# Kernel tuning notes

Measured on AMD Instinct MI355X. Metric: run time of the kernel, lower is better.

The kernel has to match this reference:

```python
import jax, jax.numpy as jnp
import numpy as np

N, E, G = 50000, 800000, 64
IN, H, ED, OUT = 32, 96, 16, 128
EPS_GEN = 1e-7   # GENConv message eps
EPS_BN = 1e-5    # BatchNorm1d eps


def _bn(x, g, b):
    # training-mode BatchNorm1d: batch stats, biased variance
    mu = jnp.mean(x, axis=0)
    var = jnp.var(x, axis=0)
    return (x - mu) * jax.lax.rsqrt(var + EPS_BN) * g + b


def _genconv(x_src, x_dst, src, dst, ea, mw1, mg, mb, mw2):
    # message: relu(x_j + e_ij) + eps            [E, H]
    msg = jax.nn.relu(x_src[src] + ea) + EPS_GEN
    n = x_dst.shape[0]
    # softmax aggregation over incoming edges per dst node (t=1.0)
    m = jax.ops.segment_max(msg, dst, num_segments=n)
    ex = jnp.exp(msg - m[dst])
    s = jax.ops.segment_sum(ex, dst, num_segments=n)
    agg = jax.ops.segment_sum(msg * (ex / s[dst]), dst, num_segments=n)
    h = agg + x_dst
    # GENConv internal MLP: Lin(H,2H,no bias) -> BN -> ReLU -> Lin(2H,H,no bias)
    h = jax.nn.relu(_bn(h @ mw1, mg, mb))
    return h @ mw2


def _forward(x, edge_attr, w_src1, w_dst1, w_edge1,
             mlp1_w1, mlp1_g, mlp1_b, mlp1_w2, bn1_g, bn1_b,
             w_edge2, mlp2_w1, mlp2_g, mlp2_b, mlp2_w2, bn2_g, bn2_b,
             w_edge3, mlp3_w1, mlp3_g, mlp3_b, mlp3_w2, bn3_g, bn3_b,
             lin_w, lin_b, edge_index, batch):
    src, dst = edge_index[0], edge_index[1]
    h = _genconv(x @ w_src1, x @ w_dst1, src, dst, edge_attr @ w_edge1,
                 mlp1_w1, mlp1_g, mlp1_b, mlp1_w2)
    h = jax.nn.relu(_bn(h, bn1_g, bn1_b))
    h = _genconv(h, h, src, dst, edge_attr @ w_edge2,
                 mlp2_w1, mlp2_g, mlp2_b, mlp2_w2)
    h = jax.nn.relu(_bn(h, bn2_g, bn2_b))
    h = _genconv(h, h, src, dst, edge_attr @ w_edge3,
                 mlp3_w1, mlp3_g, mlp3_b, mlp3_w2)
    h = jax.nn.relu(_bn(h, bn3_g, bn3_b))
    # global mean pool over graphs (dropout is identity in eval)
    cnt = jax.ops.segment_sum(jnp.ones((h.shape[0],), h.dtype), batch, num_segments=G)
    pooled = jax.ops.segment_sum(h, batch, num_segments=G) / jnp.maximum(cnt, 1.0)[:, None]
    return pooled @ lin_w + lin_b


def setup_inputs() -> dict:
    key = jax.random.key(0)
    ks = jax.random.split(key, 20)
    rn = lambda i, shp, s=0.05: jax.random.normal(ks[i], shp, jnp.float32) * s
    return {
        'x': rn(0, (N, IN), 1.0),
        'edge_attr': rn(1, (E, ED), 1.0),
        'edge_index': jax.random.randint(ks[2], (2, E), 0, N, jnp.int32),
        'batch': jnp.sort(jax.random.randint(ks[3], (N,), 0, G, jnp.int32)),
        'w_src1': rn(4, (IN, H)), 'w_dst1': rn(5, (IN, H)), 'w_edge1': rn(6, (ED, H)),
        'mlp1_w1': rn(7, (H, 2 * H)), 'mlp1_g': jnp.ones(2 * H), 'mlp1_b': jnp.zeros(2 * H),
        'mlp1_w2': rn(8, (2 * H, H)), 'bn1_g': jnp.ones(H), 'bn1_b': jnp.zeros(H),
        'w_edge2': rn(9, (ED, H)),
        'mlp2_w1': rn(10, (H, 2 * H)), 'mlp2_g': jnp.ones(2 * H), 'mlp2_b': jnp.zeros(2 * H),
        'mlp2_w2': rn(11, (2 * H, H)), 'bn2_g': jnp.ones(H), 'bn2_b': jnp.zeros(H),
        'w_edge3': rn(12, (ED, H)),
        'mlp3_w1': rn(13, (H, 2 * H)), 'mlp3_g': jnp.ones(2 * H), 'mlp3_b': jnp.zeros(2 * H),
        'mlp3_w2': rn(14, (2 * H, H)), 'bn3_g': jnp.ones(H), 'bn3_b': jnp.zeros(H),
        'lin_w': rn(15, (H, OUT)), 'lin_b': jnp.zeros(OUT),
    }


def reference(x, edge_attr, edge_index, batch, w_src1, w_dst1, w_edge1,
              mlp1_w1, mlp1_g, mlp1_b, mlp1_w2, bn1_g, bn1_b,
              w_edge2, mlp2_w1, mlp2_g, mlp2_b, mlp2_w2, bn2_g, bn2_b,
              w_edge3, mlp3_w1, mlp3_g, mlp3_b, mlp3_w2, bn3_g, bn3_b,
              lin_w, lin_b):
    return _forward(x, edge_attr, w_src1, w_dst1, w_edge1,
                    mlp1_w1, mlp1_g, mlp1_b, mlp1_w2, bn1_g, bn1_b,
                    w_edge2, mlp2_w1, mlp2_g, mlp2_b, mlp2_w2, bn2_g, bn2_b,
                    w_edge3, mlp3_w1, mlp3_g, mlp3_b, mlp3_w2, bn3_g, bn3_b,
                    lin_w, lin_b, edge_index, batch)
```

## Files before the change

### kernel.cpp

```cpp
#include <hip/hip_runtime.h>
#include <math.h>

#define NN 50000
#define EE 800000
#define GG 64
#define HH 96
#define H2 192
#define INF 32
#define EDF 16
#define OUTF 128
#define EPS_GEN 1e-7f
#define EPS_BN 1e-5f
#define NPB 100
#define NB_SCAN 49
#define NBH (256 * NB_SCAN)
#define BSCAN_PT 13
#define LOG2E 1.44269504088896f
#define SHIFT2 28.85390081777927f

typedef _Float16 f16;
typedef _Float16 f16x2 __attribute__((ext_vector_type(2)));
typedef _Float16 f16x8 __attribute__((ext_vector_type(8)));
typedef float f32x4 __attribute__((ext_vector_type(4)));

static inline size_t align256(size_t x) { return (x + 255) & ~(size_t)255; }

__device__ __forceinline__ float fdot2(f16x2 a, f16x2 b, float c) {
#if __has_builtin(__builtin_amdgcn_fdot2)
    return __builtin_amdgcn_fdot2(a, b, c, false);
#else
    return fmaf((float)a.x, (float)b.x, fmaf((float)a.y, (float)b.y, c));
#endif
}

__device__ __forceinline__ float exp2fast(float x) {
#if __has_builtin(__builtin_amdgcn_exp2f)
    return __builtin_amdgcn_exp2f(x);
#else
    return exp2f(x);
#endif
}

union W8 { float4 f[2]; f16x2 h[8]; };
union EAu { float4 f; f16x2 h[4]; };
union XUu { float2 f; f16x2 h[2]; };

__device__ __forceinline__ void agg_step(const EAu& e0, const EAu& e1, const XUu& xu,
                                         const W8* w, float* num, float* den) {
    float xv[4] = {(float)xu.h[0].x, (float)xu.h[0].y, (float)xu.h[1].x, (float)xu.h[1].y};
    #pragma unroll
    for (int cc = 0; cc < 4; ++cc) {
        float acc = 0.f;
        #pragma unroll
        for (int k = 0; k < 4; ++k) acc = fdot2(e0.h[k], w[cc].h[k], acc);
        #pragma unroll
        for (int k = 0; k < 4; ++k) acc = fdot2(e1.h[k], w[cc].h[4 + k], acc);
        float msg = fmaxf(xv[cc] + acc, 0.f) + EPS_GEN;
        float p = exp2fast(fmaf(msg, LOG2E, -SHIFT2));
        den[cc] += p;
        num[cc] = fmaf(msg, p, num[cc]);
    }
}


__global__ __launch_bounds__(256) void hist_kernel(const int* __restrict__ dst,
                                                   int* __restrict__ deg) {
    int e = blockIdx.x * 256 + threadIdx.x;
    if (e >= EE) return;
    atomicAdd(&deg[dst[e]], 1);
}

__global__ __launch_bounds__(1024) void scan1_kernel(const int* __restrict__ deg,
                                                     int* __restrict__ offs,
                                                     int* __restrict__ bsum,
                                                     int* __restrict__ bhist) {
    __shared__ int ws[16];
    __shared__ int lh[256];
    int tid = threadIdx.x, lane = tid & 63, w = tid >> 6;
    if (tid < 256) lh[tid] = 0;
    int i = blockIdx.x * 1024 + tid;
    int v = (i < NN) ? deg[i] : 0;
    __syncthreads();
    if (i < NN) {
        int b = 255 - (v > 255 ? 255 : v);
        atomicAdd(&lh[b], 1);
    }
    int x = v;
    #pragma unroll
    for (int off = 1; off < 64; off <<= 1) {
        int y = __shfl_up(x, off, 64);
        if (lane >= off) x += y;
    }
    if (lane == 63) ws[w] = x;
    __syncthreads();
    int wpre = 0;
    for (int j = 0; j < w; ++j) wpre += ws[j];
    if (i < NN) offs[i] = wpre + x - v;
    if (tid == 1023) bsum[blockIdx.x] = wpre + x;
    if (tid < 256) bhist[tid * NB_SCAN + blockIdx.x] = lh[tid];
}

__global__ __launch_bounds__(1024) void bscan_kernel(int* __restrict__ bhist,
// ... 30 lines not shown
    }
    if (lane == 63) ws[w] = x;
    __syncthreads();
    int wpre = 0;
    for (int j = 0; j < w; ++j) wpre += ws[j];
    int pre = wpre + x - s;
    #pragma unroll
    for (int i = 0; i < BSCAN_PT; ++i) {
        int idx = base + i;
        if (idx < NBH) bhist[idx] = pre + loc[i];
    }
}

__global__ __launch_bounds__(1024) void finsort_kernel(int* __restrict__ offs,
                                                       const int* __restrict__ bsum,
                                                       const int* __restrict__ deg,
                                                       const int* __restrict__ bhist,
                                                       int* __restrict__ perm) {
    __shared__ int cnt[256];
    int tid = threadIdx.x;
    if (tid < 256) cnt[tid] = 0;
    __syncthreads();
    int n = blockIdx.x * 1024 + tid;
    if (n < NN) {
        offs[n] += bsum[blockIdx.x];
        int d = deg[n];
        int b = 255 - (d > 255 ? 255 : d);
        int rank = atomicAdd(&cnt[b], 1);
        perm[bhist[b * NB_SCAN + blockIdx.x] + rank] = n;
    }
    if (n == NN) offs[NN] = EE;
}

__global__ __launch_bounds__(256) void scatter_kernel(const int* __restrict__ src,
                                                      const int* __restrict__ dst,
                                                      const int* __restrict__ offs,
                                                      int* __restrict__ cnt2,
                                                      const float* __restrict__ eattr,
                                                      int* __restrict__ csr_src,
                                                      float4* __restrict__ csrea) {
    int e = blockIdx.x * 256 + threadIdx.x;
    if (e >= EE) return;
    int d = dst[e];
    int slot = offs[d] + atomicAdd(&cnt2[d], 1);
    csr_src[slot] = src[e];
    const float4* ep = (const float4*)(eattr + (size_t)e * EDF);
    float4 v0 = ep[0], v1 = ep[1], v2 = ep[2], v3 = ep[3];
    union { f16x2 h[4]; float4 f; } a, b;
    a.h[0] = f16x2{(f16)v0.x, (f16)v0.y};
    a.h[1] = f16x2{(f16)v0.z, (f16)v0.w};
    a.h[2] = f16x2{(f16)v1.x, (f16)v1.y};
    a.h[3] = f16x2{(f16)v1.z, (f16)v1.w};
    b.h[0] = f16x2{(f16)v2.x, (f16)v2.y};
    b.h[1] = f16x2{(f16)v2.z, (f16)v2.w};
    b.h[2] = f16x2{(f16)v3.x, (f16)v3.y};
    b.h[3] = f16x2{(f16)v3.z, (f16)v3.w};
    csrea[(size_t)slot * 2] = a.f;
    csrea[(size_t)slot * 2 + 1] = b.f;
}

__global__ __launch_bounds__(256) void wprep_kernel(
    const float* __restrict__ we0, const float* __restrict__ we1, const float* __restrict__ we2,
    const float* __restrict__ m10, const float* __restrict__ m11, const float* __restrict__ m12,
    const float* __restrict__ m20, const float* __restrict__ m21, const float* __restrict__ m22,
    f16* __restrict__ wte, f16* __restrict__ wt1, f16* __restrict__ wt2,
    int* __restrict__ csr_src) {
    int idx = blockIdx.x * 256 + threadIdx.x;
    if (idx < 8) csr_src[EE + idx] = 0;
    if (idx < 4608) {
        const float* w = (idx < 1536) ? we0 : ((idx < 3072) ? we1 : we2);
        int r = idx % 1536, c = r / EDF, k = r % EDF;
        wte[idx] = (f16)w[k * HH + c];
    } else if (idx < 4608 + 3 * 18432) {
        int m = idx - 4608;
        const float* w = (m < 18432) ? m10 : ((m < 36864) ? m11 : m12);
        int r = m % 18432, j = r / HH, k = r % HH;
        wt1[m] = (f16)w[k * H2 + j];
    } else if (idx < 4608 + 6 * 18432) {
        int m = idx - 4608 - 3 * 18432;
        const float* w = (m < 18432) ? m20 : ((m < 36864) ? m21 : m22);
        int r = m % 18432, j = r / H2, k = r % H2;
        wt2[m] = (f16)w[k * HH + j];
    }
}


__global__ __launch_bounds__(256) void proj_kernel(const float* __restrict__ x,
                                                   const float* __restrict__ ws,
                                                   const float* __restrict__ wd,
                                                   f16* __restrict__ xs,
                                                   f16* __restrict__ xd) {
    __shared__ float Ws[INF * HH], Wd[INF * HH];
    int tid = threadIdx.x;
    for (int i = tid; i < INF * HH; i += 256) { Ws[i] = ws[i]; Wd[i] = wd[i]; }
    __syncthreads();
    int gid = blockIdx.x * 256 + tid;
    if (gid >= NN * HH) return;
    int n = gid / HH, c = gid % HH;
    const float* xr = x + (size_t)n * INF;
    float as = 0.f, ad = 0.f;
    #pragma unroll
    for (int k = 0; k < INF; ++k) {
        float xv = xr[k];
        as = fmaf(xv, Ws[k * HH + c], as);
        ad = fmaf(xv, Wd[k * HH + c], ad);
    }
    xs[gid] = (f16)as;
    xd[gid] = (f16)ad;
}


#define AGG_LOAD(E0, E1, XU, JJ, SR)                                    \
    E0.f = csrea[(size_t)(JJ) * 2];                                     \
    E1.f = csrea[(size_t)(JJ) * 2 + 1];                                 \
    XU.f = *(const float2*)(xsrc + (size_t)(SR) * HH + c0);

__global__ __launch_bounds__(192) void agg_kernel(const f16* __restrict__ xsrc,
                                                  const f16* __restrict__ xdst,
                                                  const float4* __restrict__ csrea,
                                                  const f16* __restrict__ wt,
                                                  const int* __restrict__ offs,
                                                  const int* __restrict__ csr_src,
                                                  const int* __restrict__ perm,
                                                  float* __restrict__ stats,
                                                  f16* __restrict__ hpre) {
    int tid = threadIdx.x;
    if (blockIdx.x == 0) {
        for (int t = tid; t < 576; t += 192) stats[t] = 0.f;
    }
    int idx = blockIdx.x * 8 + tid / 24;
    if (idx >= NN) return;
    int node = perm[idx];
    int cg = tid % 24, c0 = cg * 4;
    W8 w[4];
    #pragma unroll
    for (int cc = 0; cc < 4; ++cc) {
        const float4* wp = (const float4*)(wt + (c0 + cc) * EDF);
        w[cc].f[0] = wp[0];
        w[cc].f[1] = wp[1];
    }
    XUu xd;
    xd.f = *(const float2*)(xdst + (size_t)node * HH + c0);
    int s0 = offs[node], s1 = offs[node + 1];
    float num[4] = {0.f, 0.f, 0.f, 0.f}, den[4] = {0.f, 0.f, 0.f, 0.f};
    if (s0 < s1) {
        int last = s1 - 1;
        EAu eA0, eA1, eB0, eB1, eC0, eC1;
        XUu xA, xB, xC;
        int sA = csr_src[s0], sB = csr_src[s0 + 1], sC = csr_src[s0 + 2];
        AGG_LOAD(eA0, eA1, xA, s0, sA)
        AGG_LOAD(eB0, eB1, xB, s0 + 1, sB)
        AGG_LOAD(eC0, eC1, xC, s0 + 2, sC)
        int sD = csr_src[s0 + 3], sE = csr_src[s0 + 4], sF = csr_src[s0 + 5];
        for (int j = s0; j < s1; j += 3) {
            agg_step(eA0, eA1, xA, w, num, den);
            AGG_LOAD(eA0, eA1, xA, j + 3, sD)
            sD = csr_src[j + 6];
            if (j + 1 <= last) agg_step(eB0, eB1, xB, w, num, den);
            AGG_LOAD(eB0, eB1, xB, j + 4, sE)
            sE = csr_src[j + 7];
            if (j + 2 <= last) agg_step(eC0, eC1, xC, w, num, den);
            AGG_LOAD(eC0, eC1, xC, j + 5, sF)
            sF = csr_src[j + 8];
        }
    }
    float xdv[4] = {(float)xd.h[0].x, (float)xd.h[0].y, (float)xd.h[1].x, (float)xd.h[1].y};
    float r0 = (den[0] > 0.f) ? num[0] / den[0] : 0.f;
    float r1 = (den[1] > 0.f) ? num[1] / den[1] : 0.f;
    float r2 = (den[2] > 0.f) ? num[2] / den[2] : 0.f;
    float r3 = (den[3] > 0.f) ? num[3] / den[3] : 0.f;
    union { float2 f; f16x2 h[2]; } o;
    o.h[0] = f16x2{(f16)(r0 + xdv[0]), (f16)(r1 + xdv[1])};
    o.h[1] = f16x2{(f16)(r2 + xdv[2]), (f16)(r3 + xdv[3])};
    *(float2*)(hpre + (size_t)node * HH + c0) = o.f;
}

#define LDA1 104

__global__ __launch_bounds__(256) void gemm1_kernel(const f16* __restrict__ A,
                                                    const f16* __restrict__ Wt,
                                                    f16* __restrict__ T,
                                                    float* __restrict__ colsum,
                                                    float* __restrict__ colsumsq) {
    __shared__ f16 Al[64 * LDA1];
    __shared__ f16 Wl[192 * LDA1];
    __shared__ float red[H2 * 2];
    int tid = threadIdx.x, n0 = blockIdx.x * 64;
    for (int v = tid; v < 64 * 12; v += 256) {
        int r = v / 12, c8 = (v % 12) * 8;
        float4 d = {0.f, 0.f, 0.f, 0.f};
        if (n0 + r < NN) d = *(const float4*)(A + (size_t)(n0 + r) * HH + c8);
        *(float4*)(Al + r * LDA1 + c8) = d;
    }
    for (int v = tid; v < 192 * 12; v += 256) {
        int r = v / 12, c8 = (v % 12) * 8;
        *(float4*)(Wl + r * LDA1 + c8) = *(const float4*)(Wt + r * HH + c8);
    }
    if (tid < H2) { red[tid] = 0.f; red[H2 + tid] = 0.f; }
    __syncthreads();
    int wv = tid >> 6, l = tid & 63, lr = l & 15, lg = l >> 4;
    int i0 = wv * 16;
    f32x4 acc[12];
    #pragma unroll
    for (int t = 0; t < 12; ++t) acc[t] = (f32x4){0.f, 0.f, 0.f, 0.f};
    #pragma unroll
    for (int ks = 0; ks < 3; ++ks) {
        int k0 = ks * 32 + lg * 8;
        f16x8 af = *(const f16x8*)(Al + (i0 + lr) * LDA1 + k0);
        #pragma unroll
        for (int t = 0; t < 12; ++t) {
            f16x8 bf = *(const f16x8*)(Wl + (t * 16 + lr) * LDA1 + k0);
            acc[t] = __builtin_amdgcn_mfma_f32_16x16x32_f16(af, bf, acc[t], 0, 0, 0);
        }
    }
    #pragma unroll
    for (int t = 0; t < 12; ++t) {
        int col = t * 16 + lr;
        float s = 0.f, q = 0.f;
        #pragma unroll
        for (int rr = 0; rr < 4; ++rr) {
            int row = n0 + i0 + lg * 4 + rr;
            float v = acc[t][rr];
            if (row < NN) {
                T[(size_t)row * H2 + col] = (f16)v;
                s += v;
                q = fmaf(v, v, q);
            }
        }
        s += __shfl_xor(s, 16); s += __shfl_xor(s, 32);
        q += __shfl_xor(q, 16); q += __shfl_xor(q, 32);
        if (lg == 0) { atomicAdd(&red[col], s); atomicAdd(&red[H2 + col], q); }
    }
    __syncthreads();
    if (tid < H2) {
        atomicAdd(&colsum[tid], red[tid]);
        atomicAdd(&colsumsq[tid], red[H2 + tid]);
    }
}

#define LDA2 200

__global__ __launch_bounds__(256) void gemm2_kernel(const f16* __restrict__ T,
                                                    const f16* __restrict__ Wt,
                                                    const float* __restrict__ cs1,
                                                    const float* __restrict__ cq1,
                                                    const float* __restrict__ g1,
                                                    const float* __restrict__ b1,
                                                    f16* __restrict__ U,
                                                    float* __restrict__ colsum,
                                                    float* __restrict__ colsumsq) {
    __shared__ f16 Al[64 * LDA2];
    __shared__ f16 Wl[96 * LDA2];
    __shared__ float ab[H2 * 2];
    __shared__ float red[HH * 2];
    int tid = threadIdx.x, n0 = blockIdx.x * 64;
    if (tid < H2) {
        const float invN = 1.f / (float)NN;
        float mu = cs1[tid] * invN;
        float var = fmaxf(cq1[tid] * invN - mu * mu, 0.f);
        float a = g1[tid] * rsqrtf(var + EPS_BN);
        ab[tid] = a;
        ab[H2 + tid] = b1[tid] - mu * a;
    }
    if (tid < HH) { red[tid] = 0.f; red[HH + tid] = 0.f; }
    __syncthreads();
    for (int v = tid; v < 64 * 24; v += 256) {
        int r = v / 24, c8 = (v % 24) * 8;
        float4 dd = {0.f, 0.f, 0.f, 0.f};
        if (n0 + r < NN) {
            union { float4 f; f16x2 h[4]; } u, o;
            u.f = *(const float4*)(T + (size_t)(n0 + r) * H2 + c8);
            #pragma unroll
            for (int p = 0; p < 4; ++p) {
                float x0 = fmaxf(fmaf((float)u.h[p].x, ab[c8 + 2 * p], ab[H2 + c8 + 2 * p]), 0.f);
                float x1 = fmaxf(fmaf((float)u.h[p].y, ab[c8 + 2 * p + 1], ab[H2 + c8 + 2 * p + 1]), 0.f);
                o.h[p] = f16x2{(f16)x0, (f16)x1};
            }
            dd = o.f;
        }
        *(float4*)(Al + r * LDA2 + c8) = dd;
    }
    for (int v = tid; v < 96 * 24; v += 256) {
        int r = v / 24, c8 = (v % 24) * 8;
        *(float4*)(Wl + r * LDA2 + c8) = *(const float4*)(Wt + r * H2 + c8);
    }
    __syncthreads();
    int wv = tid >> 6, l = tid & 63, lr = l & 15, lg = l >> 4;
    int i0 = wv * 16;
    f32x4 acc[6];
    #pragma unroll
    for (int t = 0; t < 6; ++t) acc[t] = (f32x4){0.f, 0.f, 0.f, 0.f};
    #pragma unroll
    for (int ks = 0; ks < 6; ++ks) {
        int k0 = ks * 32 + lg * 8;
        f16x8 af = *(const f16x8*)(Al + (i0 + lr) * LDA2 + k0);
        #pragma unroll
        for (int t = 0; t < 6; ++t) {
            f16x8 bf = *(const f16x8*)(Wl + (t * 16 + lr) * LDA2 + k0);
            acc[t] = __builtin_amdgcn_mfma_f32_16x16x32_f16(af, bf, acc[t], 0, 0, 0);
        }
    }
    #pragma unroll
    for (int t = 0; t < 6; ++t) {
        int col = t * 16 + lr;
        float s = 0.f, q = 0.f;
        #pragma unroll
        for (int rr = 0; rr < 4; ++rr) {
            int row = n0 + i0 + lg * 4 + rr;
            float v = acc[t][rr];
            if (row < NN) {
                U[(size_t)row * HH + col] = (f16)v;
                s += v;
                q = fmaf(v, v, q);
            }
        }
        s += __shfl_xor(s, 16); s += __shfl_xor(s, 32);
        q += __shfl_xor(q, 16); q += __shfl_xor(q, 32);
        if (lg == 0) { atomicAdd(&red[col], s); atomicAdd(&red[HH + col], q); }
    }
    __syncthreads();
    if (tid < HH) {
        atomicAdd(&colsum[tid], red[tid]);
        atomicAdd(&colsumsq[tid], red[HH + tid]);
    }
}


__global__ __launch_bounds__(256) void elem_kernel(const f16* __restrict__ U,
                                                   const float* __restrict__ cs2,
                                                   const float* __restrict__ cq2,
                                                   const float* __restrict__ g2,
                                                   const float* __restrict__ b2,
                                                   f16* __restrict__ Hout) {
    __shared__ float ab[HH * 2];
    int tid = threadIdx.x;
    if (tid < HH) {
        const float invN = 1.f / (float)NN;
        float mu = cs2[tid] * invN;
        float var = fmaxf(cq2[tid] * invN - mu * mu, 0.f);
        float a = g2[tid] * rsqrtf(var + EPS_BN);
        ab[tid] = a;
        ab[HH + tid] = b2[tid] - mu * a;
    }
    __syncthreads();
    int i = blockIdx.x * 256 + tid;
    if (i >= NN * HH / 8) return;
    union { float4 f; f16x2 h[4]; } u, o;
    u.f = ((const float4*)U)[i];
    int k = (i % 12) * 8;
    #pragma unroll
    for (int p = 0; p < 4; ++p) {
        float x0 = fmaxf(fmaf((float)u.h[p].x, ab[k + 2 * p], ab[HH + k + 2 * p]), 0.f);
        float x1 = fmaxf(fmaf((float)u.h[p].y, ab[k + 2 * p + 1], ab[HH + k + 2 * p + 1]), 0.f);
// ... 54 lines not shown
    float inv = 1.f / fmaxf((float)(lo - s), 1.f);
    float acc = lb[o];
    for (int c = 0; c < HH; ++c) acc = fmaf(pool[g * HH + c] * inv, lw[c * OUTF + o], acc);
    out[(size_t)g * OUTF + o] = acc;
}


extern "C" void kernel_launch(void* const* d_in, const int* in_sizes, int n_in,
                              void* d_out, int out_size, void* d_ws, size_t ws_size,
                              hipStream_t stream) {
    const float* x = (const float*)d_in[0];
    const float* eattr = (const float*)d_in[1];
    const int* eidx = (const int*)d_in[2];
    const int* batch = (const int*)d_in[3];
    const float* w_src1 = (const float*)d_in[4];
    const float* w_dst1 = (const float*)d_in[5];
    const float* w_e[3] = {(const float*)d_in[6], (const float*)d_in[13], (const float*)d_in[20]};
    const float* mw1[3] = {(const float*)d_in[7], (const float*)d_in[14], (const float*)d_in[21]};
    const float* mg[3] = {(const float*)d_in[8], (const float*)d_in[15], (const float*)d_in[22]};
    const float* mb[3] = {(const float*)d_in[9], (const float*)d_in[16], (const float*)d_in[23]};
    const float* mw2[3] = {(const float*)d_in[10], (const float*)d_in[17], (const float*)d_in[24]};
    const float* bng[3] = {(const float*)d_in[11], (const float*)d_in[18], (const float*)d_in[25]};
    const float* bnb[3] = {(const float*)d_in[12], (const float*)d_in[19], (const float*)d_in[26]};
    const float* lin_w = (const float*)d_in[27];
    const float* lin_b = (const float*)d_in[28];
    float* out = (float*)d_out;

    const int* src = eidx;
    const int* dst = eidx + EE;

    char* base = (char*)d_ws;
    size_t off = 0;
    int* deg = (int*)(base + off); off = align256(off + (size_t)NN * 4);
    int* cnt2 = (int*)(base + off); off = align256(off + (size_t)NN * 4);
    size_t degcnt_span = off;
    int* offs = (int*)(base + off); off = align256(off + (size_t)(NN + 1) * 4);
    int* bsum = (int*)(base + off); off = align256(off + (size_t)NB_SCAN * 4);
    int* bhist = (int*)(base + off); off = align256(off + (size_t)NBH * 4);
    int* perm = (int*)(base + off); off = align256(off + (size_t)NN * 4);
    int* csr_src = (int*)(base + off); off = align256(off + (size_t)(EE + 8) * 4);
    float* stats = (float*)(base + off); off = align256(off + 576 * 4);
    float* colsum1 = stats;
    float* colsumsq1 = stats + 192;
    float* colsum2 = stats + 384;
    float* colsumsq2 = stats + 480;
    float* pool = (float*)(base + off); off = align256(off + (size_t)GG * HH * 4);
    f16* wte = (f16*)(base + off); off = align256(off + (size_t)3 * 1536 * 2);
    f16* wt1 = (f16*)(base + off); off = align256(off + (size_t)3 * 18432 * 2);
    f16* wt2 = (f16*)(base + off); off = align256(off + (size_t)3 * 18432 * 2);
    f16* XS = (f16*)(base + off); off = align256(off + (size_t)NN * HH * 2);
    f16* XD = (f16*)(base + off); off = align256(off + (size_t)NN * HH * 2);
    f16* HP = (f16*)(base + off); off = align256(off + (size_t)NN * HH * 2);
    f16* T = (f16*)(base + off); off = align256(off + (size_t)NN * H2 * 2);
    float4* csrea = (float4*)(base + off); off = align256(off + (size_t)(EE + 8) * 32);
    (void)in_sizes; (void)n_in; (void)out_size; (void)ws_size;

    hipMemsetAsync(deg, 0, degcnt_span, stream);
    hist_kernel<<<(EE + 255) / 256, 256, 0, stream>>>(dst, deg);
    scan1_kernel<<<NB_SCAN, 1024, 0, stream>>>(deg, offs, bsum, bhist);
    bscan_kernel<<<1, 1024, 0, stream>>>(bhist, bsum, pool);
    finsort_kernel<<<NB_SCAN, 1024, 0, stream>>>(offs, bsum, deg, bhist, perm);
    scatter_kernel<<<(EE + 255) / 256, 256, 0, stream>>>(src, dst, offs, cnt2, eattr,
                                                         csr_src, csrea);
    wprep_kernel<<<(4608 + 6 * 18432 + 255) / 256, 256, 0, stream>>>(
        w_e[0], w_e[1], w_e[2], mw1[0], mw1[1], mw1[2], mw2[0], mw2[1], mw2[2],
        wte, wt1, wt2, csr_src);

    proj_kernel<<<(NN * HH + 255) / 256, 256, 0, stream>>>(x, w_src1, w_dst1, XS, XD);

    for (int l = 0; l < 3; ++l) {
        const f16* xdst = (l == 0) ? XD : XS;
        agg_kernel<<<(NN + 7) / 8, 192, 0, stream>>>(XS, xdst, csrea, wte + l * 1536, offs,
                                                     csr_src, perm, stats, HP);
        gemm1_kernel<<<(NN + 63) / 64, 256, 0, stream>>>(HP, wt1 + l * 18432, T,
                                                         colsum1, colsumsq1);
        gemm2_kernel<<<(NN + 63) / 64, 256, 0, stream>>>(T, wt2 + l * 18432, colsum1,
                                                         colsumsq1, mg[l], mb[l], HP,
                                                         colsum2, colsumsq2);
        if (l < 2)
            elem_kernel<<<(NN * HH / 8 + 255) / 256, 256, 0, stream>>>(HP, colsum2, colsumsq2,
                                                                       bng[l], bnb[l], XS);
    }

    pool_bn_kernel<<<(NN + NPB - 1) / NPB, 192, 0, stream>>>(HP, colsum2, colsumsq2,
                                                             bng[2], bnb[2], batch, pool);
    out_kernel<<<GG, 128, 0, stream>>>(pool, batch, lin_w, lin_b, out);
}
```

Baseline: 566.8 us.

## Merge prep kernels, persist GEMM blocks, and raise priority in aggregation

Folds the scatter, weight-prep and input-projection kernels into one launch that splits work by block range, which removes two kernel launches. gemm1 and gemm2 now run as persistent grids of 512 blocks that loop over 64-row tiles. This loads each weight tile into shared memory once per block and makes far fewer global atomic stat flushes. The aggregation loop raises wave priority around its compute steps to interleave better with memory loads. The risks are lower parallelism in the GEMMs and extra barriers per tile.

```diff
diff --git a/kernel.cpp b/kernel.cpp
--- a/kernel.cpp
+++ b/kernel.cpp
@@ -17,6 +17,11 @@
 #define BSCAN_PT 13
 #define LOG2E 1.44269504088896f
 #define SHIFT2 28.85390081777927f
+#define GRIDP 512
+#define NT64 ((NN + 63) / 64)
+#define SCAT_BLKS 3125
+#define WPREP_BLKS 450
+#define PROJ_BLKS 18750
 
 typedef _Float16 f16;
 typedef _Float16 f16x2 __attribute__((ext_vector_type(2)));
@@ -164,81 +169,71 @@
     if (n == NN) offs[NN] = EE;
 }
 
-__global__ __launch_bounds__(256) void scatter_kernel(const int* __restrict__ src,
-                                                      const int* __restrict__ dst,
-                                                      const int* __restrict__ offs,
-                                                      int* __restrict__ cnt2,
-                                                      const float* __restrict__ eattr,
-                                                      int* __restrict__ csr_src,
-                                                      float4* __restrict__ csrea) {
-    int e = blockIdx.x * 256 + threadIdx.x;
-    if (e >= EE) return;
-    int d = dst[e];
-    int slot = offs[d] + atomicAdd(&cnt2[d], 1);
-    csr_src[slot] = src[e];
-    const float4* ep = (const float4*)(eattr + (size_t)e * EDF);
-    float4 v0 = ep[0], v1 = ep[1], v2 = ep[2], v3 = ep[3];
-    union { f16x2 h[4]; float4 f; } a, b;
-    a.h[0] = f16x2{(f16)v0.x, (f16)v0.y};
-    a.h[1] = f16x2{(f16)v0.z, (f16)v0.w};
-    a.h[2] = f16x2{(f16)v1.x, (f16)v1.y};
-    a.h[3] = f16x2{(f16)v1.z, (f16)v1.w};
-    b.h[0] = f16x2{(f16)v2.x, (f16)v2.y};
-    b.h[1] = f16x2{(f16)v2.z, (f16)v2.w};
-    b.h[2] = f16x2{(f16)v3.x, (f16)v3.y};
-    b.h[3] = f16x2{(f16)v3.z, (f16)v3.w};
-    csrea[(size_t)slot * 2] = a.f;
-    csrea[(size_t)slot * 2 + 1] = b.f;
-}
-
-__global__ __launch_bounds__(256) void wprep_kernel(
+
+__global__ __launch_bounds__(256) void prep_kernel(
+    const int* __restrict__ src, const int* __restrict__ dst,
+    const int* __restrict__ offs, int* __restrict__ cnt2,
+    const float* __restrict__ eattr, int* __restrict__ csr_src, float4* __restrict__ csrea,
     const float* __restrict__ we0, const float* __restrict__ we1, const float* __restrict__ we2,
     const float* __restrict__ m10, const float* __restrict__ m11, const float* __restrict__ m12,
     const float* __restrict__ m20, const float* __restrict__ m21, const float* __restrict__ m22,
     f16* __restrict__ wte, f16* __restrict__ wt1, f16* __restrict__ wt2,
-    int* __restrict__ csr_src) {
-    int idx = blockIdx.x * 256 + threadIdx.x;
-    if (idx < 8) csr_src[EE + idx] = 0;
-    if (idx < 4608) {
-        const float* w = (idx < 1536) ? we0 : ((idx < 3072) ? we1 : we2);
-        int r = idx % 1536, c = r / EDF, k = r % EDF;
-        wte[idx] = (f16)w[k * HH + c];
-    } else if (idx < 4608 + 3 * 18432) {
-        int m = idx - 4608;
-        const float* w = (m < 18432) ? m10 : ((m < 36864) ? m11 : m12);
-        int r = m % 18432, j = r / HH, k = r % HH;
-        wt1[m] = (f16)w[k * H2 + j];
-    } else if (idx < 4608 + 6 * 18432) {
-        int m = idx - 4608 - 3 * 18432;
-        const float* w = (m < 18432) ? m20 : ((m < 36864) ? m21 : m22);
-        int r = m % 18432, j = r / H2, k = r % H2;
-        wt2[m] = (f16)w[k * HH + j];
-    }
-}
-
-
-__global__ __launch_bounds__(256) void proj_kernel(const float* __restrict__ x,
-                                                   const float* __restrict__ ws,
-                                                   const float* __restrict__ wd,
-                                                   f16* __restrict__ xs,
-                                                   f16* __restrict__ xd) {
+    const float* __restrict__ x, const float* __restrict__ wsrc, const float* __restrict__ wdst,
+    f16* __restrict__ xs, f16* __restrict__ xd) {
     __shared__ float Ws[INF * HH], Wd[INF * HH];
-    int tid = threadIdx.x;
-    for (int i = tid; i < INF * HH; i += 256) { Ws[i] = ws[i]; Wd[i] = wd[i]; }
-    __syncthreads();
-    int gid = blockIdx.x * 256 + tid;
-    if (gid >= NN * HH) return;
-    int n = gid / HH, c = gid % HH;
-    const float* xr = x + (size_t)n * INF;
-    float as = 0.f, ad = 0.f;
-    #pragma unroll
-    for (int k = 0; k < INF; ++k) {
-        float xv = xr[k];
-        as = fmaf(xv, Ws[k * HH + c], as);
-        ad = fmaf(xv, Wd[k * HH + c], ad);
-    }
-    xs[gid] = (f16)as;
-    xd[gid] = (f16)ad;
+    int blk = blockIdx.x, tid = threadIdx.x;
+    if (blk < SCAT_BLKS) {
+        int e = blk * 256 + tid;
+        int d = dst[e];
+        int slot = offs[d] + atomicAdd(&cnt2[d], 1);
+        csr_src[slot] = src[e];
+        const float4* ep = (const float4*)(eattr + (size_t)e * EDF);
+        float4 v0 = ep[0], v1 = ep[1], v2 = ep[2], v3 = ep[3];
+        union { f16x2 h[4]; float4 f; } a, b;
+        a.h[0] = f16x2{(f16)v0.x, (f16)v0.y};
+        a.h[1] = f16x2{(f16)v0.z, (f16)v0.w};
+        a.h[2] = f16x2{(f16)v1.x, (f16)v1.y};
+        a.h[3] = f16x2{(f16)v1.z, (f16)v1.w};
+        b.h[0] = f16x2{(f16)v2.x, (f16)v2.y};
+        b.h[1] = f16x2{(f16)v2.z, (f16)v2.w};
+        b.h[2] = f16x2{(f16)v3.x, (f16)v3.y};
+        b.h[3] = f16x2{(f16)v3.z, (f16)v3.w};
+        csrea[(size_t)slot * 2] = a.f;
+        csrea[(size_t)slot * 2 + 1] = b.f;
+    } else if (blk < SCAT_BLKS + WPREP_BLKS) {
+        int idx = (blk - SCAT_BLKS) * 256 + tid;
+        if (idx < 8) csr_src[EE + idx] = 0;
+        if (idx < 4608) {
+            const float* w = (idx < 1536) ? we0 : ((idx < 3072) ? we1 : we2);
+            int r = idx % 1536, c = r / EDF, k = r % EDF;
+            wte[idx] = (f16)w[k * HH + c];
+        } else if (idx < 4608 + 3 * 18432) {
+            int m = idx - 4608;
+            const float* w = (m < 18432) ? m10 : ((m < 36864) ? m11 : m12);
+            int r = m % 18432, j = r / HH, k = r % HH;
+            wt1[m] = (f16)w[k * H2 + j];
+        } else {
+            int m = idx - 4608 - 3 * 18432;
+            const float* w = (m < 18432) ? m20 : ((m < 36864) ? m21 : m22);
+            int r = m % 18432, j = r / H2, k = r % H2;
+            wt2[m] = (f16)w[k * HH + j];
+        }
+    } else {
+        for (int i = tid; i < INF * HH; i += 256) { Ws[i] = wsrc[i]; Wd[i] = wdst[i]; }
+        __syncthreads();
+        int gid = (blk - SCAT_BLKS - WPREP_BLKS) * 256 + tid;
+        int n = gid / HH, c = gid % HH;
+        const float* xr = x + (size_t)n * INF;
+        float as = 0.f, ad = 0.f;
+        #pragma unroll
+        for (int k = 0; k < INF; ++k) {
+            float xv = xr[k];
+            as = fmaf(xv, Ws[k * HH + c], as);
+            ad = fmaf(xv, Wd[k * HH + c], ad);
+        }
+        xs[gid] = (f16)as;
+        xd[gid] = (f16)ad;
+    }
 }
 
 
@@ -285,13 +280,23 @@
         AGG_LOAD(eC0, eC1, xC, s0 + 2, sC)
         int sD = csr_src[s0 + 3], sE = csr_src[s0 + 4], sF = csr_src[s0 + 5];
         for (int j = s0; j < s1; j += 3) {
+            __builtin_amdgcn_s_setprio(1);
             agg_step(eA0, eA1, xA, w, num, den);
+            __builtin_amdgcn_s_setprio(0);
             AGG_LOAD(eA0, eA1, xA, j + 3, sD)
             sD = csr_src[j + 6];
-            if (j + 1 <= last) agg_step(eB0, eB1, xB, w, num, den);
+            if (j + 1 <= last) {
+                __builtin_amdgcn_s_setprio(1);
+                agg_step(eB0, eB1, xB, w, num, den);
+                __builtin_amdgcn_s_setprio(0);
+            }
             AGG_LOAD(eB0, eB1, xB, j + 4, sE)
             sE = csr_src[j + 7];
-            if (j + 2 <= last) agg_step(eC0, eC1, xC, w, num, den);
+            if (j + 2 <= last) {
+                __builtin_amdgcn_s_setprio(1);
+                agg_step(eC0, eC1, xC, w, num, den);
+                __builtin_amdgcn_s_setprio(0);
+            }
             AGG_LOAD(eC0, eC1, xC, j + 5, sF)
             sF = csr_src[j + 8];
         }
@@ -317,53 +322,57 @@
     __shared__ f16 Al[64 * LDA1];
     __shared__ f16 Wl[192 * LDA1];
     __shared__ float red[H2 * 2];
-    int tid = threadIdx.x, n0 = blockIdx.x * 64;
-    for (int v = tid; v < 64 * 12; v += 256) {
-        int r = v / 12, c8 = (v % 12) * 8;
-        float4 d = {0.f, 0.f, 0.f, 0.f};
-        if (n0 + r < NN) d = *(const float4*)(A + (size_t)(n0 + r) * HH + c8);
-        *(float4*)(Al + r * LDA1 + c8) = d;
-    }
+    int tid = threadIdx.x;
     for (int v = tid; v < 192 * 12; v += 256) {
         int r = v / 12, c8 = (v % 12) * 8;
         *(float4*)(Wl + r * LDA1 + c8) = *(const float4*)(Wt + r * HH + c8);
     }
-    if (tid < H2) { red[tid] = 0.f; red[H2 + tid] = 0.f; }
+    for (int t = tid; t < H2 * 2; t += 256) red[t] = 0.f;
     __syncthreads();
     int wv = tid >> 6, l = tid & 63, lr = l & 15, lg = l >> 4;
     int i0 = wv * 16;
-    f32x4 acc[12];
-    #pragma unroll
-    for (int t = 0; t < 12; ++t) acc[t] = (f32x4){0.f, 0.f, 0.f, 0.f};
-    #pragma unroll
-    for (int ks = 0; ks < 3; ++ks) {
-        int k0 = ks * 32 + lg * 8;
-        f16x8 af = *(const f16x8*)(Al + (i0 + lr) * LDA1 + k0);
+    for (int tile = blockIdx.x; tile < NT64; tile += GRIDP) {
+        int n0 = tile * 64;
+        for (int v = tid; v < 64 * 12; v += 256) {
+            int r = v / 12, c8 = (v % 12) * 8;
+            float4 d = {0.f, 0.f, 0.f, 0.f};
+            if (n0 + r < NN) d = *(const float4*)(A + (size_t)(n0 + r) * HH + c8);
+            *(float4*)(Al + r * LDA1 + c8) = d;
+        }
+        __syncthreads();
+        f32x4 acc[12];
+        #pragma unroll
+        for (int t = 0; t < 12; ++t) acc[t] = (f32x4){0.f, 0.f, 0.f, 0.f};
+        #pragma unroll
+        for (int ks = 0; ks < 3; ++ks) {
+            int k0 = ks * 32 + lg * 8;
+            f16x8 af = *(const f16x8*)(Al + (i0 + lr) * LDA1 + k0);
+            #pragma unroll
+            for (int t = 0; t < 12; ++t) {
+                f16x8 bf = *(const f16x8*)(Wl + (t * 16 + lr) * LDA1 + k0);
+                acc[t] = __builtin_amdgcn_mfma_f32_16x16x32_f16(af, bf, acc[t], 0, 0, 0);
+            }
+        }
         #pragma unroll
         for (int t = 0; t < 12; ++t) {
-            f16x8 bf = *(const f16x8*)(Wl + (t * 16 + lr) * LDA1 + k0);
-            acc[t] = __builtin_amdgcn_mfma_f32_16x16x32_f16(af, bf, acc[t], 0, 0, 0);
-        }
-    }
-    #pragma unroll
-    for (int t = 0; t < 12; ++t) {
-        int col = t * 16 + lr;
-        float s = 0.f, q = 0.f;
-        #pragma unroll
-        for (int rr = 0; rr < 4; ++rr) {
-            int row = n0 + i0 + lg * 4 + rr;
-            float v = acc[t][rr];
-            if (row < NN) {
-                T[(size_t)row * H2 + col] = (f16)v;
-                s += v;
-                q = fmaf(v, v, q);
+            int col = t * 16 + lr;
+            float s = 0.f, q = 0.f;
+            #pragma unroll
+            for (int rr = 0; rr < 4; ++rr) {
+                int row = n0 + i0 + lg * 4 + rr;
+                float v = acc[t][rr];
+                if (row < NN) {
+                    T[(size_t)row * H2 + col] = (f16)v;
+                    s += v;
+                    q = fmaf(v, v, q);
+                }
             }
-        }
-        s += __shfl_xor(s, 16); s += __shfl_xor(s, 32);
-        q += __shfl_xor(q, 16); q += __shfl_xor(q, 32);
-        if (lg == 0) { atomicAdd(&red[col], s); atomicAdd(&red[H2 + col], q); }
-    }
-    __syncthreads();
+            s += __shfl_xor(s, 16); s += __shfl_xor(s, 32);
+            q += __shfl_xor(q, 16); q += __shfl_xor(q, 32);
+            if (lg == 0) { atomicAdd(&red[col], s); atomicAdd(&red[H2 + col], q); }
+        }
+        __syncthreads();
+    }
     if (tid < H2) {
         atomicAdd(&colsum[tid], red[tid]);
         atomicAdd(&colsumsq[tid], red[H2 + tid]);
@@ -385,7 +394,7 @@
     __shared__ f16 Wl[96 * LDA2];
     __shared__ float ab[H2 * 2];
     __shared__ float red[HH * 2];
-    int tid = threadIdx.x, n0 = blockIdx.x * 64;
+    int tid = threadIdx.x;
     if (tid < H2) {
         const float invN = 1.f / (float)NN;
         float mu = cs1[tid] * invN;
@@ -394,24 +403,7 @@
         ab[tid] = a;
         ab[H2 + tid] = b1[tid] - mu * a;
     }
-    if (tid < HH) { red[tid] = 0.f; red[HH + tid] = 0.f; }
-    __syncthreads();
-    for (int v = tid; v < 64 * 24; v += 256) {
-        int r = v / 24, c8 = (v % 24) * 8;
-        float4 dd = {0.f, 0.f, 0.f, 0.f};
-        if (n0 + r < NN) {
-            union { float4 f; f16x2 h[4]; } u, o;
-            u.f = *(const float4*)(T + (size_t)(n0 + r) * H2 + c8);
-            #pragma unroll
-            for (int p = 0; p < 4; ++p) {
-                float x0 = fmaxf(fmaf((float)u.h[p].x, ab[c8 + 2 * p], ab[H2 + c8 + 2 * p]), 0.f);
-                float x1 = fmaxf(fmaf((float)u.h[p].y, ab[c8 + 2 * p + 1], ab[H2 + c8 + 2 * p + 1]), 0.f);
-                o.h[p] = f16x2{(f16)x0, (f16)x1};
-            }
-            dd = o.f;
-        }
-        *(float4*)(Al + r * LDA2 + c8) = dd;
-    }
+    if (tid < HH * 2) red[tid] = 0.f;
     for (int v = tid; v < 96 * 24; v += 256) {
         int r = v / 24, c8 = (v % 24) * 8;
         *(float4*)(Wl + r * LDA2 + c8) = *(const float4*)(Wt + r * H2 + c8);
@@ -419,38 +411,58 @@
     __syncthreads();
     int wv = tid >> 6, l = tid & 63, lr = l & 15, lg = l >> 4;
     int i0 = wv * 16;
-    f32x4 acc[6];
-    #pragma unroll
-    for (int t = 0; t < 6; ++t) acc[t] = (f32x4){0.f, 0.f, 0.f, 0.f};
-    #pragma unroll
-    for (int ks = 0; ks < 6; ++ks) {
-        int k0 = ks * 32 + lg * 8;
-        f16x8 af = *(const f16x8*)(Al + (i0 + lr) * LDA2 + k0);
+    for (int tile = blockIdx.x; tile < NT64; tile += GRIDP) {
+        int n0 = tile * 64;
+        for (int v = tid; v < 64 * 24; v += 256) {
+            int r = v / 24, c8 = (v % 24) * 8;
+            float4 dd = {0.f, 0.f, 0.f, 0.f};
+            if (n0 + r < NN) {
+                union { float4 f; f16x2 h[4]; } u, o;
+                u.f = *(const float4*)(T + (size_t)(n0 + r) * H2 + c8);
+                #pragma unroll
+                for (int p = 0; p < 4; ++p) {
+                    float x0 = fmaxf(fmaf((float)u.h[p].x, ab[c8 + 2 * p], ab[H2 + c8 + 2 * p]), 0.f);
+                    float x1 = fmaxf(fmaf((float)u.h[p].y, ab[c8 + 2 * p + 1], ab[H2 + c8 + 2 * p + 1]), 0.f);
+                    o.h[p] = f16x2{(f16)x0, (f16)x1};
+                }
+                dd = o.f;
+            }
+            *(float4*)(Al + r * LDA2 + c8) = dd;
+        }
+        __syncthreads();
+        f32x4 acc[6];
+        #pragma unroll
+        for (int t = 0; t < 6; ++t) acc[t] = (f32x4){0.f, 0.f, 0.f, 0.f};
+        #pragma unroll
+        for (int ks = 0; ks < 6; ++ks) {
+            int k0 = ks * 32 + lg * 8;
+            f16x8 af = *(const f16x8*)(Al + (i0 + lr) * LDA2 + k0);
+            #pragma unroll
+            for (int t = 0; t < 6; ++t) {
+                f16x8 bf = *(const f16x8*)(Wl + (t * 16 + lr) * LDA2 + k0);
+                acc[t] = __builtin_amdgcn_mfma_f32_16x16x32_f16(af, bf, acc[t], 0, 0, 0);
+            }
+        }
         #pragma unroll
         for (int t = 0; t < 6; ++t) {
-            f16x8 bf = *(const f16x8*)(Wl + (t * 16 + lr) * LDA2 + k0);
-            acc[t] = __builtin_amdgcn_mfma_f32_16x16x32_f16(af, bf, acc[t], 0, 0, 0);
-        }
-    }
-    #pragma unroll
-    for (int t = 0; t < 6; ++t) {
-        int col = t * 16 + lr;
-        float s = 0.f, q = 0.f;
-        #pragma unroll
-        for (int rr = 0; rr < 4; ++rr) {
-            int row = n0 + i0 + lg * 4 + rr;
-            float v = acc[t][rr];
-            if (row < NN) {
-                U[(size_t)row * HH + col] = (f16)v;
-                s += v;
-                q = fmaf(v, v, q);
+            int col = t * 16 + lr;
+            float s = 0.f, q = 0.f;
+            #pragma unroll
+            for (int rr = 0; rr < 4; ++rr) {
+                int row = n0 + i0 + lg * 4 + rr;
+                float v = acc[t][rr];
+                if (row < NN) {
+                    U[(size_t)row * HH + col] = (f16)v;
+                    s += v;
+                    q = fmaf(v, v, q);
+                }
             }
-        }
-        s += __shfl_xor(s, 16); s += __shfl_xor(s, 32);
-        q += __shfl_xor(q, 16); q += __shfl_xor(q, 32);
-        if (lg == 0) { atomicAdd(&red[col], s); atomicAdd(&red[HH + col], q); }
-    }
-    __syncthreads();
+            s += __shfl_xor(s, 16); s += __shfl_xor(s, 32);
+            q += __shfl_xor(q, 16); q += __shfl_xor(q, 32);
+            if (lg == 0) { atomicAdd(&red[col], s); atomicAdd(&red[HH + col], q); }
+        }
+        __syncthreads();
+    }
     if (tid < HH) {
         atomicAdd(&colsum[tid], red[tid]);
         atomicAdd(&colsumsq[tid], red[HH + tid]);
@@ -599,23 +611,18 @@
     scan1_kernel<<<NB_SCAN, 1024, 0, stream>>>(deg, offs, bsum, bhist);
     bscan_kernel<<<1, 1024, 0, stream>>>(bhist, bsum, pool);
     finsort_kernel<<<NB_SCAN, 1024, 0, stream>>>(offs, bsum, deg, bhist, perm);
-    scatter_kernel<<<(EE + 255) / 256, 256, 0, stream>>>(src, dst, offs, cnt2, eattr,
-                                                         csr_src, csrea);
-    wprep_kernel<<<(4608 + 6 * 18432 + 255) / 256, 256, 0, stream>>>(
+    prep_kernel<<<SCAT_BLKS + WPREP_BLKS + PROJ_BLKS, 256, 0, stream>>>(
+        src, dst, offs, cnt2, eattr, csr_src, csrea,
         w_e[0], w_e[1], w_e[2], mw1[0], mw1[1], mw1[2], mw2[0], mw2[1], mw2[2],
-        wte, wt1, wt2, csr_src);
-
-    proj_kernel<<<(NN * HH + 255) / 256, 256, 0, stream>>>(x, w_src1, w_dst1, XS, XD);
+        wte, wt1, wt2, x, w_src1, w_dst1, XS, XD);
 
     for (int l = 0; l < 3; ++l) {
         const f16* xdst = (l == 0) ? XD : XS;
         agg_kernel<<<(NN + 7) / 8, 192, 0, stream>>>(XS, xdst, csrea, wte + l * 1536, offs,
                                                      csr_src, perm, stats, HP);
-        gemm1_kernel<<<(NN + 63) / 64, 256, 0, stream>>>(HP, wt1 + l * 18432, T,
-                                                         colsum1, colsumsq1);
-        gemm2_kernel<<<(NN + 63) / 64, 256, 0, stream>>>(T, wt2 + l * 18432, colsum1,
-                                                         colsumsq1, mg[l], mb[l], HP,
-                                                         colsum2, colsumsq2);
+        gemm1_kernel<<<GRIDP, 256, 0, stream>>>(HP, wt1 + l * 18432, T, colsum1, colsumsq1);
+        gemm2_kernel<<<GRIDP, 256, 0, stream>>>(T, wt2 + l * 18432, colsum1, colsumsq1,
+                                                mg[l], mb[l], HP, colsum2, colsumsq2);
         if (l < 2)
             elem_kernel<<<(NN * HH / 8 + 255) / 256, 256, 0, stream>>>(HP, colsum2, colsumsq2,
                                                                        bng[l], bnb[l], XS);
```

New measurement: 512.3 us. 9.6% less time.

## Persistent GEMM grids, reuse hist atomic ranks in scatter, raise agg compute priority

Applied to the files above, without the earlier changes.

The histogram kernel now stores each edge's atomic rank, so the scatter kernel no longer needs a second per-node atomic counter or its memset. Both GEMM kernels become persistent with a fixed grid of 512 blocks that loop over 64-row tiles. The weight tile is loaded into LDS once per block and the column statistics are reduced once per block, which cuts the number of global atomics. The aggregation loop wraps its compute steps in s_setprio so loads overlap better. In exchange it adds an 800K-int rank buffer plus an extra write and read of it, and it uses fewer GEMM blocks.

```diff
diff --git a/kernel.cpp b/kernel.cpp
--- a/kernel.cpp
+++ b/kernel.cpp
@@ -17,6 +17,8 @@
 #define BSCAN_PT 13
 #define LOG2E 1.44269504088896f
 #define SHIFT2 28.85390081777927f
+#define GRIDP 512
+#define NT64 ((NN + 63) / 64)
 
 typedef _Float16 f16;
 typedef _Float16 f16x2 __attribute__((ext_vector_type(2)));
@@ -64,10 +66,11 @@
 
 
 __global__ __launch_bounds__(256) void hist_kernel(const int* __restrict__ dst,
-                                                   int* __restrict__ deg) {
+                                                   int* __restrict__ deg,
+                                                   int* __restrict__ rank) {
     int e = blockIdx.x * 256 + threadIdx.x;
     if (e >= EE) return;
-    atomicAdd(&deg[dst[e]], 1);
+    rank[e] = atomicAdd(&deg[dst[e]], 1);
 }
 
 __global__ __launch_bounds__(1024) void scan1_kernel(const int* __restrict__ deg,
@@ -167,14 +170,14 @@
 __global__ __launch_bounds__(256) void scatter_kernel(const int* __restrict__ src,
                                                       const int* __restrict__ dst,
                                                       const int* __restrict__ offs,
-                                                      int* __restrict__ cnt2,
+                                                      const int* __restrict__ rank,
                                                       const float* __restrict__ eattr,
                                                       int* __restrict__ csr_src,
                                                       float4* __restrict__ csrea) {
     int e = blockIdx.x * 256 + threadIdx.x;
     if (e >= EE) return;
     int d = dst[e];
-    int slot = offs[d] + atomicAdd(&cnt2[d], 1);
+    int slot = offs[d] + rank[e];
     csr_src[slot] = src[e];
     const float4* ep = (const float4*)(eattr + (size_t)e * EDF);
     float4 v0 = ep[0], v1 = ep[1], v2 = ep[2], v3 = ep[3];
@@ -285,13 +288,23 @@
         AGG_LOAD(eC0, eC1, xC, s0 + 2, sC)
         int sD = csr_src[s0 + 3], sE = csr_src[s0 + 4], sF = csr_src[s0 + 5];
         for (int j = s0; j < s1; j += 3) {
+            __builtin_amdgcn_s_setprio(1);
             agg_step(eA0, eA1, xA, w, num, den);
+            __builtin_amdgcn_s_setprio(0);
             AGG_LOAD(eA0, eA1, xA, j + 3, sD)
             sD = csr_src[j + 6];
-            if (j + 1 <= last) agg_step(eB0, eB1, xB, w, num, den);
+            if (j + 1 <= last) {
+                __builtin_amdgcn_s_setprio(1);
+                agg_step(eB0, eB1, xB, w, num, den);
+                __builtin_amdgcn_s_setprio(0);
+            }
             AGG_LOAD(eB0, eB1, xB, j + 4, sE)
             sE = csr_src[j + 7];
-            if (j + 2 <= last) agg_step(eC0, eC1, xC, w, num, den);
+            if (j + 2 <= last) {
+                __builtin_amdgcn_s_setprio(1);
+                agg_step(eC0, eC1, xC, w, num, den);
+                __builtin_amdgcn_s_setprio(0);
+            }
             AGG_LOAD(eC0, eC1, xC, j + 5, sF)
             sF = csr_src[j + 8];
         }
@@ -317,53 +330,57 @@
     __shared__ f16 Al[64 * LDA1];
     __shared__ f16 Wl[192 * LDA1];
     __shared__ float red[H2 * 2];
-    int tid = threadIdx.x, n0 = blockIdx.x * 64;
-    for (int v = tid; v < 64 * 12; v += 256) {
-        int r = v / 12, c8 = (v % 12) * 8;
-        float4 d = {0.f, 0.f, 0.f, 0.f};
-        if (n0 + r < NN) d = *(const float4*)(A + (size_t)(n0 + r) * HH + c8);
-        *(float4*)(Al + r * LDA1 + c8) = d;
-    }
+    int tid = threadIdx.x;
     for (int v = tid; v < 192 * 12; v += 256) {
         int r = v / 12, c8 = (v % 12) * 8;
         *(float4*)(Wl + r * LDA1 + c8) = *(const float4*)(Wt + r * HH + c8);
     }
-    if (tid < H2) { red[tid] = 0.f; red[H2 + tid] = 0.f; }
+    for (int t = tid; t < H2 * 2; t += 256) red[t] = 0.f;
     __syncthreads();
     int wv = tid >> 6, l = tid & 63, lr = l & 15, lg = l >> 4;
     int i0 = wv * 16;
-    f32x4 acc[12];
-    #pragma unroll
-    for (int t = 0; t < 12; ++t) acc[t] = (f32x4){0.f, 0.f, 0.f, 0.f};
-    #pragma unroll
-    for (int ks = 0; ks < 3; ++ks) {
-        int k0 = ks * 32 + lg * 8;
-        f16x8 af = *(const f16x8*)(Al + (i0 + lr) * LDA1 + k0);
+    for (int tile = blockIdx.x; tile < NT64; tile += GRIDP) {
+        int n0 = tile * 64;
+        for (int v = tid; v < 64 * 12; v += 256) {
+            int r = v / 12, c8 = (v % 12) * 8;
+            float4 d = {0.f, 0.f, 0.f, 0.f};
+            if (n0 + r < NN) d = *(const float4*)(A + (size_t)(n0 + r) * HH + c8);
+            *(float4*)(Al + r * LDA1 + c8) = d;
+        }
+        __syncthreads();
+        f32x4 acc[12];
+        #pragma unroll
+        for (int t = 0; t < 12; ++t) acc[t] = (f32x4){0.f, 0.f, 0.f, 0.f};
+        #pragma unroll
+        for (int ks = 0; ks < 3; ++ks) {
+            int k0 = ks * 32 + lg * 8;
+            f16x8 af = *(const f16x8*)(Al + (i0 + lr) * LDA1 + k0);
+            #pragma unroll
+            for (int t = 0; t < 12; ++t) {
+                f16x8 bf = *(const f16x8*)(Wl + (t * 16 + lr) * LDA1 + k0);
+                acc[t] = __builtin_amdgcn_mfma_f32_16x16x32_f16(af, bf, acc[t], 0, 0, 0);
+            }
+        }
         #pragma unroll
         for (int t = 0; t < 12; ++t) {
-            f16x8 bf = *(const f16x8*)(Wl + (t * 16 + lr) * LDA1 + k0);
-            acc[t] = __builtin_amdgcn_mfma_f32_16x16x32_f16(af, bf, acc[t], 0, 0, 0);
-        }
-    }
-    #pragma unroll
-    for (int t = 0; t < 12; ++t) {
-        int col = t * 16 + lr;
-        float s = 0.f, q = 0.f;
-        #pragma unroll
-        for (int rr = 0; rr < 4; ++rr) {
-            int row = n0 + i0 + lg * 4 + rr;
-            float v = acc[t][rr];
-            if (row < NN) {
-                T[(size_t)row * H2 + col] = (f16)v;
-                s += v;
-                q = fmaf(v, v, q);
+            int col = t * 16 + lr;
+            float s = 0.f, q = 0.f;
+            #pragma unroll
+            for (int rr = 0; rr < 4; ++rr) {
+                int row = n0 + i0 + lg * 4 + rr;
+                float v = acc[t][rr];
+                if (row < NN) {
+                    T[(size_t)row * H2 + col] = (f16)v;
+                    s += v;
+                    q = fmaf(v, v, q);
+                }
             }
-        }
-        s += __shfl_xor(s, 16); s += __shfl_xor(s, 32);
-        q += __shfl_xor(q, 16); q += __shfl_xor(q, 32);
-        if (lg == 0) { atomicAdd(&red[col], s); atomicAdd(&red[H2 + col], q); }
-    }
-    __syncthreads();
+            s += __shfl_xor(s, 16); s += __shfl_xor(s, 32);
+            q += __shfl_xor(q, 16); q += __shfl_xor(q, 32);
+            if (lg == 0) { atomicAdd(&red[col], s); atomicAdd(&red[H2 + col], q); }
+        }
+        __syncthreads();
+    }
     if (tid < H2) {
         atomicAdd(&colsum[tid], red[tid]);
         atomicAdd(&colsumsq[tid], red[H2 + tid]);
@@ -385,7 +402,7 @@
     __shared__ f16 Wl[96 * LDA2];
     __shared__ float ab[H2 * 2];
     __shared__ float red[HH * 2];
-    int tid = threadIdx.x, n0 = blockIdx.x * 64;
+    int tid = threadIdx.x;
     if (tid < H2) {
         const float invN = 1.f / (float)NN;
         float mu = cs1[tid] * invN;
@@ -394,24 +411,7 @@
         ab[tid] = a;
         ab[H2 + tid] = b1[tid] - mu * a;
     }
-    if (tid < HH) { red[tid] = 0.f; red[HH + tid] = 0.f; }
-    __syncthreads();
-    for (int v = tid; v < 64 * 24; v += 256) {
-        int r = v / 24, c8 = (v % 24) * 8;
-        float4 dd = {0.f, 0.f, 0.f, 0.f};
-        if (n0 + r < NN) {
-            union { float4 f; f16x2 h[4]; } u, o;
-            u.f = *(const float4*)(T + (size_t)(n0 + r) * H2 + c8);
-            #pragma unroll
-            for (int p = 0; p < 4; ++p) {
-                float x0 = fmaxf(fmaf((float)u.h[p].x, ab[c8 + 2 * p], ab[H2 + c8 + 2 * p]), 0.f);
-                float x1 = fmaxf(fmaf((float)u.h[p].y, ab[c8 + 2 * p + 1], ab[H2 + c8 + 2 * p + 1]), 0.f);
-                o.h[p] = f16x2{(f16)x0, (f16)x1};
-            }
-            dd = o.f;
-        }
-        *(float4*)(Al + r * LDA2 + c8) = dd;
-    }
+    if (tid < HH * 2) red[tid] = 0.f;
     for (int v = tid; v < 96 * 24; v += 256) {
         int r = v / 24, c8 = (v % 24) * 8;
         *(float4*)(Wl + r * LDA2 + c8) = *(const float4*)(Wt + r * H2 + c8);
@@ -419,38 +419,58 @@
     __syncthreads();
     int wv = tid >> 6, l = tid & 63, lr = l & 15, lg = l >> 4;
     int i0 = wv * 16;
-    f32x4 acc[6];
-    #pragma unroll
-    for (int t = 0; t < 6; ++t) acc[t] = (f32x4){0.f, 0.f, 0.f, 0.f};
-    #pragma unroll
-    for (int ks = 0; ks < 6; ++ks) {
-        int k0 = ks * 32 + lg * 8;
-        f16x8 af = *(const f16x8*)(Al + (i0 + lr) * LDA2 + k0);
+    for (int tile = blockIdx.x; tile < NT64; tile += GRIDP) {
+        int n0 = tile * 64;
+        for (int v = tid; v < 64 * 24; v += 256) {
+            int r = v / 24, c8 = (v % 24) * 8;
+            float4 dd = {0.f, 0.f, 0.f, 0.f};
+            if (n0 + r < NN) {
+                union { float4 f; f16x2 h[4]; } u, o;
+                u.f = *(const float4*)(T + (size_t)(n0 + r) * H2 + c8);
+                #pragma unroll
+                for (int p = 0; p < 4; ++p) {
+                    float x0 = fmaxf(fmaf((float)u.h[p].x, ab[c8 + 2 * p], ab[H2 + c8 + 2 * p]), 0.f);
+                    float x1 = fmaxf(fmaf((float)u.h[p].y, ab[c8 + 2 * p + 1], ab[H2 + c8 + 2 * p + 1]), 0.f);
+                    o.h[p] = f16x2{(f16)x0, (f16)x1};
+                }
+                dd = o.f;
+            }
+            *(float4*)(Al + r * LDA2 + c8) = dd;
+        }
+        __syncthreads();
+        f32x4 acc[6];
+        #pragma unroll
+        for (int t = 0; t < 6; ++t) acc[t] = (f32x4){0.f, 0.f, 0.f, 0.f};
+        #pragma unroll
+        for (int ks = 0; ks < 6; ++ks) {
+            int k0 = ks * 32 + lg * 8;
+            f16x8 af = *(const f16x8*)(Al + (i0 + lr) * LDA2 + k0);
+            #pragma unroll
+            for (int t = 0; t < 6; ++t) {
+                f16x8 bf = *(const f16x8*)(Wl + (t * 16 + lr) * LDA2 + k0);
+                acc[t] = __builtin_amdgcn_mfma_f32_16x16x32_f16(af, bf, acc[t], 0, 0, 0);
+            }
+        }
         #pragma unroll
         for (int t = 0; t < 6; ++t) {
-            f16x8 bf = *(const f16x8*)(Wl + (t * 16 + lr) * LDA2 + k0);
-            acc[t] = __builtin_amdgcn_mfma_f32_16x16x32_f16(af, bf, acc[t], 0, 0, 0);
-        }
-    }
-    #pragma unroll
-    for (int t = 0; t < 6; ++t) {
-        int col = t * 16 + lr;
-        float s = 0.f, q = 0.f;
-        #pragma unroll
-        for (int rr = 0; rr < 4; ++rr) {
-            int row = n0 + i0 + lg * 4 + rr;
-            float v = acc[t][rr];
-            if (row < NN) {
-                U[(size_t)row * HH + col] = (f16)v;
-                s += v;
-                q = fmaf(v, v, q);
+            int col = t * 16 + lr;
+            float s = 0.f, q = 0.f;
+            #pragma unroll
+            for (int rr = 0; rr < 4; ++rr) {
+                int row = n0 + i0 + lg * 4 + rr;
+                float v = acc[t][rr];
+                if (row < NN) {
+                    U[(size_t)row * HH + col] = (f16)v;
+                    s += v;
+                    q = fmaf(v, v, q);
+                }
             }
-        }
-        s += __shfl_xor(s, 16); s += __shfl_xor(s, 32);
-        q += __shfl_xor(q, 16); q += __shfl_xor(q, 32);
-        if (lg == 0) { atomicAdd(&red[col], s); atomicAdd(&red[HH + col], q); }
-    }
-    __syncthreads();
+            s += __shfl_xor(s, 16); s += __shfl_xor(s, 32);
+            q += __shfl_xor(q, 16); q += __shfl_xor(q, 32);
+            if (lg == 0) { atomicAdd(&red[col], s); atomicAdd(&red[HH + col], q); }
+        }
+        __syncthreads();
+    }
     if (tid < HH) {
         atomicAdd(&colsum[tid], red[tid]);
         atomicAdd(&colsumsq[tid], red[HH + tid]);
@@ -571,8 +591,7 @@
     char* base = (char*)d_ws;
     size_t off = 0;
     int* deg = (int*)(base + off); off = align256(off + (size_t)NN * 4);
-    int* cnt2 = (int*)(base + off); off = align256(off + (size_t)NN * 4);
-    size_t degcnt_span = off;
+    int* rank = (int*)(base + off); off = align256(off + (size_t)EE * 4);
     int* offs = (int*)(base + off); off = align256(off + (size_t)(NN + 1) * 4);
     int* bsum = (int*)(base + off); off = align256(off + (size_t)NB_SCAN * 4);
     int* bhist = (int*)(base + off); off = align256(off + (size_t)NBH * 4);
@@ -594,28 +613,25 @@
     float4* csrea = (float4*)(base + off); off = align256(off + (size_t)(EE + 8) * 32);
     (void)in_sizes; (void)n_in; (void)out_size; (void)ws_size;
 
-    hipMemsetAsync(deg, 0, degcnt_span, stream);
-    hist_kernel<<<(EE + 255) / 256, 256, 0, stream>>>(dst, deg);
+    hipMemsetAsync(deg, 0, (size_t)NN * 4, stream);
+    hist_kernel<<<(EE + 255) / 256, 256, 0, stream>>>(dst, deg, rank);
     scan1_kernel<<<NB_SCAN, 1024, 0, stream>>>(deg, offs, bsum, bhist);
     bscan_kernel<<<1, 1024, 0, stream>>>(bhist, bsum, pool);
     finsort_kernel<<<NB_SCAN, 1024, 0, stream>>>(offs, bsum, deg, bhist, perm);
-    scatter_kernel<<<(EE + 255) / 256, 256, 0, stream>>>(src, dst, offs, cnt2, eattr,
+    scatter_kernel<<<(EE + 255) / 256, 256, 0, stream>>>(src, dst, offs, rank, eattr,
                                                          csr_src, csrea);
     wprep_kernel<<<(4608 + 6 * 18432 + 255) / 256, 256, 0, stream>>>(
         w_e[0], w_e[1], w_e[2], mw1[0], mw1[1], mw1[2], mw2[0], mw2[1], mw2[2],
         wte, wt1, wt2, csr_src);
-
     proj_kernel<<<(NN * HH + 255) / 256, 256, 0, stream>>>(x, w_src1, w_dst1, XS, XD);
 
     for (int l = 0; l < 3; ++l) {
         const f16* xdst = (l == 0) ? XD : XS;
         agg_kernel<<<(NN + 7) / 8, 192, 0, stream>>>(XS, xdst, csrea, wte + l * 1536, offs,
                                                      csr_src, perm, stats, HP);
-        gemm1_kernel<<<(NN + 63) / 64, 256, 0, stream>>>(HP, wt1 + l * 18432, T,
-                                                         colsum1, colsumsq1);
-        gemm2_kernel<<<(NN + 63) / 64, 256, 0, stream>>>(T, wt2 + l * 18432, colsum1,
-                                                         colsumsq1, mg[l], mb[l], HP,
-                                                         colsum2, colsumsq2);
+        gemm1_kernel<<<GRIDP, 256, 0, stream>>>(HP, wt1 + l * 18432, T, colsum1, colsumsq1);
+        gemm2_kernel<<<GRIDP, 256, 0, stream>>>(T, wt2 + l * 18432, colsum1, colsumsq1,
+                                                mg[l], mb[l], HP, colsum2, colsumsq2);
         if (l < 2)
             elem_kernel<<<(NN * HH / 8 + 255) / 256, 256, 0, stream>>>(HP, colsum2, colsumsq2,
                                                                        bng[l], bnb[l], XS);
```

Result: faster. 505.8 us (-10.8%).
